# Performance work log

Hardware: AMD Instinct MI355X
Metric: run time of the kernel (lower is better)

## Reference

```python
import jax, jax.numpy as jnp
import numpy as np

N_NODES = 20000
N_EDGES = 640000
BASIS = 128
NUM_GAUSS = 64
HIDDEN = 256
NUM_ATOMS = 100
NUM_GRAPHS = 256
T = 3


def setup_inputs() -> dict:
    key = jax.random.key(0)
    ks = jax.random.split(key, 16)
    Z = jax.random.randint(ks[0], (N_NODES,), 0, NUM_ATOMS + 1)
    edge_index = jax.random.randint(ks[1], (2, N_EDGES), 0, N_NODES)
    edge_attr = jax.random.normal(ks[2], (N_EDGES, NUM_GAUSS), dtype=jnp.float32)
    batch = jnp.sort(jax.random.randint(ks[3], (N_NODES,), 0, NUM_GRAPHS))
    s = 0.05
    embed = jax.random.normal(ks[4], (NUM_ATOMS + 1, BASIS), dtype=jnp.float32)
    cfW = jax.random.normal(ks[5], (BASIS, BASIS), dtype=jnp.float32) * s
    cfb = jax.random.normal(ks[6], (BASIS,), dtype=jnp.float32) * s
    dfW = jax.random.normal(ks[7], (BASIS, NUM_GAUSS), dtype=jnp.float32) * s
    dfb = jax.random.normal(ks[8], (BASIS,), dtype=jnp.float32) * s
    fcW = jax.random.normal(ks[9], (BASIS, BASIS), dtype=jnp.float32) * s
    r1W = jax.random.normal(ks[10], (HIDDEN, BASIS), dtype=jnp.float32) * s
    r1b = jax.random.normal(ks[11], (HIDDEN,), dtype=jnp.float32) * s
    r2W = jax.random.normal(ks[12], (4, HIDDEN), dtype=jnp.float32) * s
    r2b = jax.random.normal(ks[13], (4,), dtype=jnp.float32) * s
    return dict(Z=Z, edge_index=edge_index, edge_attr=edge_attr, batch=batch,
                embed=embed, cfW=cfW, cfb=cfb, dfW=dfW, dfb=dfb, fcW=fcW,
                r1W=r1W, r1b=r1b, r2W=r2W, r2b=r2b)


def reference(Z, edge_index, edge_attr, batch, embed, cfW, cfb, dfW, dfb, fcW,
              r1W, r1b, r2W, r2b):
    # Node embeddings C: [N, basis]
    C = embed[Z]
    src = edge_index[0]  # x_j source nodes
    dst = edge_index[1]  # aggregation target nodes
    # df(edge_attr) is iteration-invariant (shared InteractionBlock weights)
    d_feat = edge_attr @ dfW.T + dfb  # [E, basis]
    for _ in range(T):
        # message: tanh(fc(cf(x_j) * df(edge_attr)))
        c_feat = C[src] @ cfW.T + cfb                 # [E, basis]
        m = jnp.tanh((c_feat * d_feat) @ fcW.T)       # [E, basis]
        agg = jax.ops.segment_sum(m, dst, num_segments=N_NODES)
        C = C + agg
    # readout MLP: Linear -> tanh -> Linear
    h = jnp.tanh(C @ r1W.T + r1b) @ r2W.T + r2b       # [N, 4]
    # global_add_pool over graphs
    return jax.ops.segment_sum(h, batch, num_segments=NUM_GRAPHS)  # [G, 4]
```

## Files before the change

### kernel.cpp

```cpp
#include <hip/hip_runtime.h>
#include <cstdint>

#define NN 20000
#define NE 640000
#define NB 128
#define NG 64
#define NH 256

typedef __attribute__((ext_vector_type(8))) short bf16x8;
typedef __attribute__((ext_vector_type(4))) float f32x4;
typedef __attribute__((ext_vector_type(4))) float fvec4;
typedef __attribute__((ext_vector_type(4))) unsigned uvec4;

__device__ __forceinline__ unsigned fbits(float f){ union{float f; unsigned u;} v; v.f=f; return v.u; }
__device__ __forceinline__ float ubits(unsigned u){ union{unsigned u; float f;} v; v.u=u; return v.f; }

__device__ __forceinline__ unsigned pkf(float a, float b){
  return __builtin_amdgcn_perm(fbits(b)+0x8000u, fbits(a)+0x8000u, 0x07060302u);
}
__device__ __forceinline__ unsigned mulbb(unsigned c, unsigned d){
  float lo = ubits(c << 16) * ubits(d << 16);
  float hi = ubits(c & 0xFFFF0000u) * ubits(d & 0xFFFF0000u);
  return pkf(lo, hi);
}
__device__ __forceinline__ short f2bf_fast(float f){ return (short)((fbits(f)+0x8000u)>>16); }

__device__ __forceinline__ float tanh_fast(float x){
  float t = __builtin_amdgcn_exp2f(x * 2.8853900817779268f);
  return __builtin_fmaf(-2.f, __builtin_amdgcn_rcpf(t + 1.f), 1.f);
}

template<int NT, int KT>
__device__ __forceinline__ void stage_w(const float* __restrict__ W, short* lds){
  const int total = NT*KT*64;
  for(int c = (int)threadIdx.x; c < total; c += 256){
    int lane = c & 63;
    int kt = (c >> 6) % KT;
    int n  = c / (64*KT);
    int row = n*16 + (lane & 15);
    int col = kt*32 + (lane >> 4)*8;
    const float* p = W + (size_t)row*(KT*32) + col;
    unsigned* d = (unsigned*)(lds + (size_t)c*8);
#pragma unroll
    for(int j=0;j<4;j++) d[j] = pkf(p[2*j], p[2*j+1]);
  }
}

__global__ void k_prep0(const int* __restrict__ Z, const float* __restrict__ E,
                        float* __restrict__ C, const int* __restrict__ dst, int* __restrict__ cnt){
  int i = blockIdx.x*256 + threadIdx.x;
  int node = i >> 5, k4 = i & 31;
  ((float4*)C)[i] = ((const float4*)(E + (size_t)Z[node]*NB))[k4];
  atomicAdd(&cnt[dst[i]], 1);
}

__global__ __launch_bounds__(1024) void k_scan(const int* __restrict__ cnt, int* __restrict__ cur){
  __shared__ int lds[1024];
  const int t = threadIdx.x;
  const int base = t*20;
  int4 v[5];
#pragma unroll
  for(int j=0;j<5;j++) v[j] = ((const int4*)(cnt + base))[j];
  const int* ve = (const int*)v;
  int loc[20]; int s = 0;
#pragma unroll
  for(int j=0;j<20;j++){ int c = (base+j < NN) ? ve[j] : 0; loc[j] = s; s += c; }
  lds[t] = s;
  __syncthreads();
  for(int off=1; off<1024; off<<=1){
    int x = (t >= off) ? lds[t-off] : 0;
    __syncthreads();
    lds[t] += x;
    __syncthreads();
  }
  int prefix = (t > 0) ? lds[t-1] : 0;
#pragma unroll
  for(int j=0;j<20;j++){ int i = base+j; if(i<NN) cur[i] = prefix + loc[j]; }
}

__global__ void k_fill(const int* __restrict__ src, const int* __restrict__ dst,
                       int* __restrict__ cur, int* __restrict__ perm,
                       int* __restrict__ srcv, int* __restrict__ dstv){
  int e = blockIdx.x*256 + threadIdx.x;
  if(e < NE){
    int v = dst[e];
    int p = atomicAdd(&cur[v], 1);
    perm[p] = e;
    srcv[p] = src[e];
    dstv[p] = v;
  }
}

#define TPAD 136
__global__ __launch_bounds__(256,3) void k_dprep(
  const float* __restrict__ ea, const int* __restrict__ perm,
  const float* __restrict__ dfW, const float* __restrict__ dfb, short* __restrict__ dft)
{
  __shared__ short ldsW[8*2*64*8];
  __shared__ short ldsT[4*32*TPAD];
  stage_w<8,2>(dfW, ldsW);
  __syncthreads();
  const int lane = threadIdx.x & 63, wave = threadIdx.x >> 6;
  const int quad = lane>>4, lc = lane&15;
  short* myT = ldsT + wave*32*TPAD;
  const int tile0 = (blockIdx.x*4 + wave)*2;

  float bias[8];
#pragma unroll
  for(int n2=0;n2<8;n2++) bias[n2] = dfb[n2*16 + lc];

  int eA[2], eB[2];
#pragma unroll
  for(int mt=0;mt<2;mt++){
    eA[mt] = perm[ tile0   *32 + mt*16 + lc];
    eB[mt] = perm[(tile0+1)*32 + mt*16 + lc];
  }

  fvec4 rA[2][2][2];
#pragma unroll
  for(int mt=0;mt<2;mt++){
    const float* p = ea + (size_t)eA[mt]*NG;
#pragma unroll
    for(int kt=0;kt<2;kt++){
      const float* q = p + kt*32 + quad*8;
      rA[mt][kt][0] = __builtin_nontemporal_load((const fvec4*)q);
      rA[mt][kt][1] = __builtin_nontemporal_load((const fvec4*)(q+4));
    }
  }

  f32x4 z = {0.f,0.f,0.f,0.f};

  auto convert_mfma = [&](fvec4 (&raw)[2][2][2], f32x4 (&acc)[2][8]){
#pragma unroll
    for(int mt=0;mt<2;mt++)
#pragma unroll
      for(int n2=0;n2<8;n2++) acc[mt][n2] = z;
#pragma unroll
    for(int kt=0;kt<2;kt++){
      bf16x8 a0, a1;
      {
        union{ bf16x8 v; unsigned u[4]; } t0, t1;
        fvec4 c0 = raw[0][kt][0], c1 = raw[0][kt][1];
        fvec4 d0 = raw[1][kt][0], d1 = raw[1][kt][1];
        t0.u[0]=pkf(c0.x,c0.y); t0.u[1]=pkf(c0.z,c0.w); t0.u[2]=pkf(c1.x,c1.y); t0.u[3]=pkf(c1.z,c1.w);
        t1.u[0]=pkf(d0.x,d0.y); t1.u[1]=pkf(d0.z,d0.w); t1.u[2]=pkf(d1.x,d1.y); t1.u[3]=pkf(d1.z,d1.w);
        a0 = t0.v; a1 = t1.v;
      }
#pragma unroll
      for(int n2=0;n2<8;n2++){
        bf16x8 b = *(const bf16x8*)(ldsW + ((size_t)(n2*2+kt)*64 + lane)*8);
        acc[0][n2] = __builtin_amdgcn_mfma_f32_16x16x32_bf16(a0, b, acc[0][n2], 0, 0, 0);
        acc[1][n2] = __builtin_amdgcn_mfma_f32_16x16x32_bf16(a1, b, acc[1][n2], 0, 0, 0);
      }
    }
  };

  auto store_tile = [&](f32x4 (&acc)[2][8], int tile){
#pragma unroll
    for(int n2=0;n2<8;n2++)
#pragma unroll
      for(int mt=0;mt<2;mt++)
#pragma unroll
        for(int r=0;r<4;r++)
          myT[(mt*16 + quad*4 + r)*TPAD + n2*16 + lc] = f2bf_fast(acc[mt][n2][r] + bias[n2]);
    short* gout = dft + (size_t)tile*32*NB;
#pragma unroll
    for(int i=0;i<8;i++){
      int s_ = i*512 + lane*8;
      int row = s_ >> 7, col = s_ & 127;
      uvec4 vv = *(const uvec4*)(myT + row*TPAD + col);
      __builtin_nontemporal_store(vv, (uvec4*)(gout + s_));
    }
  };

  f32x4 accA[2][8];
  convert_mfma(rA, accA);

  fvec4 rB[2][2][2];
#pragma unroll
  for(int mt=0;mt<2;mt++){
    const float* p = ea + (size_t)eB[mt]*NG;
#pragma unroll
    for(int kt=0;kt<2;kt++){
      const float* q = p + kt*32 + quad*8;
      rB[mt][kt][0] = __builtin_nontemporal_load((const fvec4*)q);
      rB[mt][kt][1] = __builtin_nontemporal_load((const fvec4*)(q+4));
    }
  }

  store_tile(accA, tile0);

  f32x4 accB[2][8];
  convert_mfma(rB, accB);
  store_tile(accB, tile0+1);
}

__global__ __launch_bounds__(256,3) void k_cf(
  const float* __restrict__ C, const float* __restrict__ cfW,
  const float* __restrict__ cfb, short* __restrict__ cfC)
{
  __shared__ short ldsW[8*4*64*8];
  __shared__ short ldsT[4*16*TPAD];
  stage_w<8,4>(cfW, ldsW);
  __syncthreads();
  const int lane = threadIdx.x & 63, wave = threadIdx.x >> 6;
  const int quad = lane>>4, lc = lane&15;
  short* myT = ldsT + wave*16*TPAD;
  const int tile = blockIdx.x*4 + wave;
  if(tile >= NN/16) return;
  const int base = tile*16;
  bf16x8 a[4];
  const float* p = C + (size_t)(base + lc)*NB;
#pragma unroll
  for(int kt=0;kt<4;kt++){
    const float* q = p + kt*32 + quad*8;
    float4 c0 = *(const float4*)q, c1 = *(const float4*)(q+4);
    union{ bf16x8 v; unsigned u[4]; } t;
    t.u[0]=pkf(c0.x,c0.y); t.u[1]=pkf(c0.z,c0.w); t.u[2]=pkf(c1.x,c1.y); t.u[3]=pkf(c1.z,c1.w);
    a[kt] = t.v;
  }
  f32x4 acc[8];
  f32x4 z = {0.f,0.f,0.f,0.f};
#pragma unroll
  for(int n2=0;n2<8;n2++) acc[n2] = z;
#pragma unroll
  for(int kt=0;kt<4;kt++)
#pragma unroll
    for(int n2=0;n2<8;n2++){
      bf16x8 b = *(const bf16x8*)(ldsW + ((size_t)(n2*4+kt)*64 + lane)*8);
      acc[n2] = __builtin_amdgcn_mfma_f32_16x16x32_bf16(a[kt], b, acc[n2], 0, 0, 0);
    }
#pragma unroll
  for(int n2=0;n2<8;n2++){
    float bias = cfb[n2*16 + lc];
#pragma unroll
    for(int r=0;r<4;r++)
      myT[(quad*4 + r)*TPAD + n2*16 + lc] = f2bf_fast(acc[n2][r] + bias);
  }
  short* gout = cfC + (size_t)base*NB;
#pragma unroll
  for(int i=0;i<4;i++){
    int s_ = i*512 + lane*8;
    int row = s_ >> 7, col = s_ & 127;
    uint4 vv = *(const uint4*)(myT + row*TPAD + col);
    *(uint4*)(gout + s_) = vv;
  }
}

#define ETPW 4
__global__ __launch_bounds__(256,2) void k_edge(
    const short* __restrict__ cfC, const short* __restrict__ dft,
    const int* __restrict__ srcv, const int* __restrict__ dstv,
    const float* __restrict__ fcW, float* __restrict__ C)
{
  __shared__ short ldsW[8*4*64*8];
  stage_w<8,4>(fcW, ldsW);
  __syncthreads();
  const int lane = threadIdx.x & 63, wave = threadIdx.x >> 6;
  const int quad = lane>>4, lc = lane&15;
  const int tile0 = (blockIdx.x*4 + wave)*ETPW;

  int   sv[2][2];
  int   dv[2];
  uint4 cc[2][2][4];
  uint4 dd[2][2][4];

  {
    const int base = tile0*32;
#pragma unroll
    for(int mt=0;mt<2;mt++) sv[0][mt] = srcv[base + mt*16 + lc];
    dv[0] = dstv[base + (lane&31)];
#pragma unroll
    for(int mt=0;mt<2;mt++){
      const short* dp = dft + (size_t)(base + mt*16 + lc)*NB;
#pragma unroll
      for(int kt=0;kt<4;kt++) dd[0][mt][kt] = *(const uint4*)(dp + kt*32 + quad*8);
    }
#pragma unroll
    for(int mt=0;mt<2;mt++){
      const short* cp = cfC + (size_t)sv[0][mt]*NB;
#pragma unroll
      for(int kt=0;kt<4;kt++) cc[0][mt][kt] = *(const uint4*)(cp + kt*32 + quad*8);
    }
  }

#pragma unroll
  for(int t=0; t<ETPW; t++){
    const int cur = t & 1, nxt = cur ^ 1;

    if(t+1 < ETPW){
      const int nbase = (tile0 + t + 1)*32;
#pragma unroll
      for(int mt=0;mt<2;mt++) sv[nxt][mt] = srcv[nbase + mt*16 + lc];
      dv[nxt] = dstv[nbase + (lane&31)];
#pragma unroll
      for(int mt=0;mt<2;mt++){
        const short* dp = dft + (size_t)(nbase + mt*16 + lc)*NB;
#pragma unroll
        for(int kt=0;kt<4;kt++) dd[nxt][mt][kt] = *(const uint4*)(dp + kt*32 + quad*8);
      }
    }

    f32x4 acc[2][8];
    f32x4 z = {0.f,0.f,0.f,0.f};
#pragma unroll
    for(int mt=0;mt<2;mt++)
#pragma unroll
      for(int n2=0;n2<8;n2++) acc[mt][n2] = z;
#pragma unroll
    for(int kt=0;kt<4;kt++){
      bf16x8 a0, a1;
      {
        union{ bf16x8 v; unsigned u[4]; } t0, t1;
        uint4 c0 = cc[cur][0][kt], d0 = dd[cur][0][kt];
        uint4 c1 = cc[cur][1][kt], d1 = dd[cur][1][kt];
        t0.u[0] = mulbb(c0.x, d0.x); t0.u[1] = mulbb(c0.y, d0.y);
        t0.u[2] = mulbb(c0.z, d0.z); t0.u[3] = mulbb(c0.w, d0.w);
        t1.u[0] = mulbb(c1.x, d1.x); t1.u[1] = mulbb(c1.y, d1.y);
        t1.u[2] = mulbb(c1.z, d1.z); t1.u[3] = mulbb(c1.w, d1.w);
        a0 = t0.v; a1 = t1.v;
      }
#pragma unroll
      for(int n2=0;n2<8;n2++){
        bf16x8 b = *(const bf16x8*)(ldsW + ((size_t)(n2*4 + kt)*64 + lane)*8);
        acc[0][n2] = __builtin_amdgcn_mfma_f32_16x16x32_bf16(a0, b, acc[0][n2], 0, 0, 0);
        acc[1][n2] = __builtin_amdgcn_mfma_f32_16x16x32_bf16(a1, b, acc[1][n2], 0, 0, 0);
      }
    }

    if(t+1 < ETPW){
#pragma unroll
      for(int mt=0;mt<2;mt++){
        const short* cp = cfC + (size_t)sv[nxt][mt]*NB;
#pragma unroll
        for(int kt=0;kt<4;kt++) cc[nxt][mt][kt] = *(const uint4*)(cp + kt*32 + quad*8);
      }
    }

#pragma unroll
    for(int mt=0;mt<2;mt++)
#pragma unroll
      for(int n2=0;n2<8;n2++)
#pragma unroll
        for(int r=0;r<4;r++) acc[mt][n2][r] = tanh_fast(acc[mt][n2][r]);

    const int i = lane & 31;
    const int di = dv[cur];
    const int dshift = __shfl_up(di, 1);
    const int dprev = (i > 0) ? dshift : -1;
    unsigned long long mm = __ballot(di != dprev) & 0xFFFFFFFFull;
    while(mm){
      int lo = __ffsll(mm) - 1;
      mm &= mm - 1;
      int hi = mm ? (__ffsll(mm) - 1) : 32;
      int v = __shfl(di, lo);
      float sums[8];
#pragma unroll
      for(int n2=0;n2<8;n2++) sums[n2] = 0.f;
#pragma unroll
      for(int mt=0; mt<2; mt++)
#pragma unroll
        for(int r=0; r<4; r++){
          int e2 = mt*16 + quad*4 + r;
          float sel = (e2 >= lo && e2 < hi) ? 1.f : 0.f;
#pragma unroll
          for(int n2=0;n2<8;n2++) sums[n2] = __builtin_fmaf(acc[mt][n2][r], sel, sums[n2]);
        }
#pragma unroll
      for(int n2=0;n2<8;n2++){
        sums[n2] += __shfl_xor(sums[n2], 16);
        sums[n2] += __shfl_xor(sums[n2], 32);
      }
      const int n2w = quad*2;
      atomicAdd(&C[(size_t)v*NB + n2w*16 + lc],     sums[n2w]);
      atomicAdd(&C[(size_t)v*NB + (n2w+1)*16 + lc], sums[n2w+1]);
    }
  }
}

__global__ __launch_bounds__(256,2) void k_readout(
  const float* __restrict__ C, const float* __restrict__ r1W, const float* __restrict__ r1b,
  const float* __restrict__ r2W, const float* __restrict__ r2b,
  const int* __restrict__ batch, float* __restrict__ out)
{
  __shared__ short ldsW[16*4*64*8];
  stage_w<16,4>(r1W, ldsW);
  __syncthreads();
  const int lane = threadIdx.x & 63, wave = threadIdx.x >> 6;
  const int quad = lane>>4, lc = lane&15;
  const int base = (blockIdx.x*4 + wave)*16;
  if(base >= NN) return;
  int node = base + lc; if(node > NN-1) node = NN-1;
  bf16x8 a[4];
  const float* p = C + (size_t)node*NB;
#pragma unroll
  for(int kt=0;kt<4;kt++){
    const float* q = p + kt*32 + quad*8;
    float4 c0 = *(const float4*)q, c1 = *(const float4*)(q+4);
    union{ bf16x8 v; unsigned u[4]; } t;
    t.u[0]=pkf(c0.x,c0.y); t.u[1]=pkf(c0.z,c0.w); t.u[2]=pkf(c1.x,c1.y); t.u[3]=pkf(c1.z,c1.w);
    a[kt] = t.v;
  }
  f32x4 acc[16];
  f32x4 z = {0.f,0.f,0.f,0.f};
#pragma unroll
  for(int nt=0;nt<16;nt++) acc[nt] = z;
#pragma unroll
  for(int kt=0;kt<4;kt++)
#pragma unroll
    for(int nt=0;nt<16;nt++){
      bf16x8 b = *(const bf16x8*)(ldsW + ((size_t)(nt*4+kt)*64 + lane)*8);
      acc[nt] = __builtin_amdgcn_mfma_f32_16x16x32_bf16(a[kt], b, acc[nt], 0, 0, 0);
    }
#pragma unroll
  for(int nt=0;nt<16;nt++){
    float bias = r1b[nt*16 + lc];
#pragma unroll
    for(int r=0;r<4;r++) acc[nt][r] = tanh_fast(acc[nt][r] + bias);
  }
#pragma unroll
  for(int r=0;r<4;r++){
    int nd = base + quad*4 + r;
#pragma unroll
    for(int o=0;o<4;o++){
      float ps = 0.f;
#pragma unroll
      for(int nt=0;nt<16;nt++) ps = __builtin_fmaf(acc[nt][r], r2W[(size_t)o*NH + nt*16 + lc], ps);
      ps += __shfl_xor(ps, 1);
      ps += __shfl_xor(ps, 2);
      ps += __shfl_xor(ps, 4);
      ps += __shfl_xor(ps, 8);
      if(lc == 0 && nd < NN) atomicAdd(&out[batch[nd]*4 + o], ps + r2b[o]);
    }
  }
}

extern "C" void kernel_launch(void* const* d_in, const int* in_sizes, int n_in,
                              void* d_out, int out_size, void* d_ws, size_t ws_size,
                              hipStream_t stream) {
  const int*   Z      = (const int*)d_in[0];
  const int*   ei     = (const int*)d_in[1];
  const float* ea     = (const float*)d_in[2];
  const int*   batch  = (const int*)d_in[3];
  const float* embedW = (const float*)d_in[4];
  const float* cfW    = (const float*)d_in[5];
  const float* cfb    = (const float*)d_in[6];
  const float* dfW    = (const float*)d_in[7];
  const float* dfb    = (const float*)d_in[8];
  const float* fcW    = (const float*)d_in[9];
  const float* r1W    = (const float*)d_in[10];
  const float* r1b    = (const float*)d_in[11];
  const float* r2W    = (const float*)d_in[12];
  const float* r2b    = (const float*)d_in[13];
  const int* src = ei;
  const int* dst = ei + NE;

  char* p = (char*)d_ws;
  auto alloc = [&](size_t b){ char* r = p; p += (b + 255) & ~(size_t)255; return r; };
  float* CA    = (float*)alloc((size_t)NN*NB*4);
  short* cfC   = (short*)alloc((size_t)NN*NB*2);
  short* dft   = (short*)alloc((size_t)NE*NB*2);
  int*   cnt   = (int*)alloc((size_t)NN*4);
  int*   cursor= (int*)alloc((size_t)NN*4);
  int*   perm  = (int*)alloc((size_t)NE*4);
  int*   srcv  = (int*)alloc((size_t)NE*4);
  int*   dstv  = (int*)alloc((size_t)NE*4);
  size_t needed = (size_t)(p - (char*)d_ws);

  (void)hipMemsetAsync(d_out, 0, (size_t)out_size*sizeof(float), stream);
  if(needed > ws_size) return;

  (void)hipMemsetAsync(cnt, 0, (size_t)NN*4, stream);
  k_prep0<<<2500, 256, 0, stream>>>(Z, embedW, CA, dst, cnt);
  k_scan <<<1,   1024, 0, stream>>>(cnt, cursor);
  k_fill <<<2500, 256, 0, stream>>>(src, dst, cursor, perm, srcv, dstv);
  k_dprep<<<2500, 256, 0, stream>>>(ea, perm, dfW, dfb, dft);

  for(int it = 0; it < 3; it++){
    k_cf  <<<313,  256, 0, stream>>>(CA, cfW, cfb, cfC);
    k_edge<<<1250, 256, 0, stream>>>(cfC, dft, srcv, dstv, fcW, CA);
  }
  k_readout<<<313, 256, 0, stream>>>(CA, r1W, r1b, r2W, r2b, batch, (float*)d_out);
}
```

Before: 666.1 us.

## Switch bf16 MFMA path to fp16 with packed multiply and merged src/dst index array

Converts all intermediate edge/node features and weights from bf16 to fp16, using the hardware pack-convert and v_pk_mul_f16 in place of the manual bf16 multiply emulation, and fp16 MFMA instructions. It also merges the separate src and dst index arrays into one int2 array loaded once per tile and redistributed with shuffles, and raises the edge kernel occupancy hint from 2 to 3 blocks. The goal is to cut ALU work in the edge message inner loop and reduce index loads. fp16 has a narrower range than bf16, so large activations could overflow.

```diff
diff --git a/kernel.cpp b/kernel.cpp
--- a/kernel.cpp
+++ b/kernel.cpp
@@ -7,23 +7,27 @@
 #define NG 64
 #define NH 256
 
-typedef __attribute__((ext_vector_type(8))) short bf16x8;
+typedef __attribute__((ext_vector_type(8))) _Float16 h16x8;
 typedef __attribute__((ext_vector_type(4))) float f32x4;
 typedef __attribute__((ext_vector_type(4))) float fvec4;
 typedef __attribute__((ext_vector_type(4))) unsigned uvec4;
 
 __device__ __forceinline__ unsigned fbits(float f){ union{float f; unsigned u;} v; v.f=f; return v.u; }
-__device__ __forceinline__ float ubits(unsigned u){ union{unsigned u; float f;} v; v.u=u; return v.f; }
-
-__device__ __forceinline__ unsigned pkf(float a, float b){
-  return __builtin_amdgcn_perm(fbits(b)+0x8000u, fbits(a)+0x8000u, 0x07060302u);
-}
-__device__ __forceinline__ unsigned mulbb(unsigned c, unsigned d){
-  float lo = ubits(c << 16) * ubits(d << 16);
-  float hi = ubits(c & 0xFFFF0000u) * ubits(d & 0xFFFF0000u);
-  return pkf(lo, hi);
-}
-__device__ __forceinline__ short f2bf_fast(float f){ return (short)((fbits(f)+0x8000u)>>16); }
+
+__device__ __forceinline__ unsigned pkh(float a, float b){
+  auto t = __builtin_amdgcn_cvt_pkrtz(a, b);
+  return __builtin_bit_cast(unsigned, t);
+}
+__device__ __forceinline__ unsigned pkh_rne(float a, float b){
+  union{ _Float16 h[2]; unsigned u; } v;
+  v.h[0] = (_Float16)a; v.h[1] = (_Float16)b; return v.u;
+}
+__device__ __forceinline__ unsigned pkmul(unsigned a, unsigned b){
+  unsigned r; asm("v_pk_mul_f16 %0, %1, %2" : "=v"(r) : "v"(a), "v"(b)); return r;
+}
+__device__ __forceinline__ short f2h(float f){
+  union{ _Float16 h[2]; short s[2]; } v; v.h[0] = (_Float16)f; return v.s[0];
+}
 
 __device__ __forceinline__ float tanh_fast(float x){
   float t = __builtin_amdgcn_exp2f(x * 2.8853900817779268f);
@@ -42,7 +46,7 @@
     const float* p = W + (size_t)row*(KT*32) + col;
     unsigned* d = (unsigned*)(lds + (size_t)c*8);
 #pragma unroll
-    for(int j=0;j<4;j++) d[j] = pkf(p[2*j], p[2*j+1]);
+    for(int j=0;j<4;j++) d[j] = pkh_rne(p[2*j], p[2*j+1]);
   }
 }
 
@@ -80,14 +84,13 @@
 
 __global__ void k_fill(const int* __restrict__ src, const int* __restrict__ dst,
                        int* __restrict__ cur, int* __restrict__ perm,
-                       int* __restrict__ srcv, int* __restrict__ dstv){
+                       int2* __restrict__ sd){
   int e = blockIdx.x*256 + threadIdx.x;
   if(e < NE){
     int v = dst[e];
     int p = atomicAdd(&cur[v], 1);
     perm[p] = e;
-    srcv[p] = src[e];
-    dstv[p] = v;
+    sd[p] = make_int2(src[e], v);
   }
 }
 
@@ -137,20 +140,20 @@
       for(int n2=0;n2<8;n2++) acc[mt][n2] = z;
 #pragma unroll
     for(int kt=0;kt<2;kt++){
-      bf16x8 a0, a1;
+      h16x8 a0, a1;
       {
-        union{ bf16x8 v; unsigned u[4]; } t0, t1;
+        union{ h16x8 v; unsigned u[4]; } t0, t1;
         fvec4 c0 = raw[0][kt][0], c1 = raw[0][kt][1];
         fvec4 d0 = raw[1][kt][0], d1 = raw[1][kt][1];
-        t0.u[0]=pkf(c0.x,c0.y); t0.u[1]=pkf(c0.z,c0.w); t0.u[2]=pkf(c1.x,c1.y); t0.u[3]=pkf(c1.z,c1.w);
-        t1.u[0]=pkf(d0.x,d0.y); t1.u[1]=pkf(d0.z,d0.w); t1.u[2]=pkf(d1.x,d1.y); t1.u[3]=pkf(d1.z,d1.w);
+        t0.u[0]=pkh(c0.x,c0.y); t0.u[1]=pkh(c0.z,c0.w); t0.u[2]=pkh(c1.x,c1.y); t0.u[3]=pkh(c1.z,c1.w);
+        t1.u[0]=pkh(d0.x,d0.y); t1.u[1]=pkh(d0.z,d0.w); t1.u[2]=pkh(d1.x,d1.y); t1.u[3]=pkh(d1.z,d1.w);
         a0 = t0.v; a1 = t1.v;
       }
 #pragma unroll
       for(int n2=0;n2<8;n2++){
-        bf16x8 b = *(const bf16x8*)(ldsW + ((size_t)(n2*2+kt)*64 + lane)*8);
-        acc[0][n2] = __builtin_amdgcn_mfma_f32_16x16x32_bf16(a0, b, acc[0][n2], 0, 0, 0);
-        acc[1][n2] = __builtin_amdgcn_mfma_f32_16x16x32_bf16(a1, b, acc[1][n2], 0, 0, 0);
+        h16x8 b = *(const h16x8*)(ldsW + ((size_t)(n2*2+kt)*64 + lane)*8);
+        acc[0][n2] = __builtin_amdgcn_mfma_f32_16x16x32_f16(a0, b, acc[0][n2], 0, 0, 0);
+        acc[1][n2] = __builtin_amdgcn_mfma_f32_16x16x32_f16(a1, b, acc[1][n2], 0, 0, 0);
       }
     }
   };
@@ -162,7 +165,7 @@
       for(int mt=0;mt<2;mt++)
 #pragma unroll
         for(int r=0;r<4;r++)
-          myT[(mt*16 + quad*4 + r)*TPAD + n2*16 + lc] = f2bf_fast(acc[mt][n2][r] + bias[n2]);
+          myT[(mt*16 + quad*4 + r)*TPAD + n2*16 + lc] = f2h(acc[mt][n2][r] + bias[n2]);
     short* gout = dft + (size_t)tile*32*NB;
 #pragma unroll
     for(int i=0;i<8;i++){
@@ -209,14 +212,14 @@
   const int tile = blockIdx.x*4 + wave;
   if(tile >= NN/16) return;
   const int base = tile*16;
-  bf16x8 a[4];
+  h16x8 a[4];
   const float* p = C + (size_t)(base + lc)*NB;
 #pragma unroll
   for(int kt=0;kt<4;kt++){
     const float* q = p + kt*32 + quad*8;
     float4 c0 = *(const float4*)q, c1 = *(const float4*)(q+4);
-    union{ bf16x8 v; unsigned u[4]; } t;
-    t.u[0]=pkf(c0.x,c0.y); t.u[1]=pkf(c0.z,c0.w); t.u[2]=pkf(c1.x,c1.y); t.u[3]=pkf(c1.z,c1.w);
+    union{ h16x8 v; unsigned u[4]; } t;
+    t.u[0]=pkh(c0.x,c0.y); t.u[1]=pkh(c0.z,c0.w); t.u[2]=pkh(c1.x,c1.y); t.u[3]=pkh(c1.z,c1.w);
     a[kt] = t.v;
   }
   f32x4 acc[8];
@@ -227,15 +230,15 @@
   for(int kt=0;kt<4;kt++)
 #pragma unroll
     for(int n2=0;n2<8;n2++){
-      bf16x8 b = *(const bf16x8*)(ldsW + ((size_t)(n2*4+kt)*64 + lane)*8);
-      acc[n2] = __builtin_amdgcn_mfma_f32_16x16x32_bf16(a[kt], b, acc[n2], 0, 0, 0);
+      h16x8 b = *(const h16x8*)(ldsW + ((size_t)(n2*4+kt)*64 + lane)*8);
+      acc[n2] = __builtin_amdgcn_mfma_f32_16x16x32_f16(a[kt], b, acc[n2], 0, 0, 0);
     }
 #pragma unroll
   for(int n2=0;n2<8;n2++){
     float bias = cfb[n2*16 + lc];
 #pragma unroll
     for(int r=0;r<4;r++)
-      myT[(quad*4 + r)*TPAD + n2*16 + lc] = f2bf_fast(acc[n2][r] + bias);
+      myT[(quad*4 + r)*TPAD + n2*16 + lc] = f2h(acc[n2][r] + bias);
   }
   short* gout = cfC + (size_t)base*NB;
 #pragma unroll
@@ -248,9 +251,9 @@
 }
 
 #define ETPW 4
-__global__ __launch_bounds__(256,2) void k_edge(
+__global__ __launch_bounds__(256,3) void k_edge(
     const short* __restrict__ cfC, const short* __restrict__ dft,
-    const int* __restrict__ srcv, const int* __restrict__ dstv,
+    const int2* __restrict__ sd,
     const float* __restrict__ fcW, float* __restrict__ C)
 {
   __shared__ short ldsW[8*4*64*8];
@@ -267,9 +270,10 @@
 
   {
     const int base = tile0*32;
-#pragma unroll
-    for(int mt=0;mt<2;mt++) sv[0][mt] = srcv[base + mt*16 + lc];
-    dv[0] = dstv[base + (lane&31)];
+    int2 s0 = sd[base + (lane&31)];
+    dv[0] = s0.y;
+    sv[0][0] = __shfl(s0.x, lc);
+    sv[0][1] = __shfl(s0.x, 16 + lc);
 #pragma unroll
     for(int mt=0;mt<2;mt++){
       const short* dp = dft + (size_t)(base + mt*16 + lc)*NB;
@@ -290,9 +294,10 @@
 
     if(t+1 < ETPW){
       const int nbase = (tile0 + t + 1)*32;
-#pragma unroll
-      for(int mt=0;mt<2;mt++) sv[nxt][mt] = srcv[nbase + mt*16 + lc];
-      dv[nxt] = dstv[nbase + (lane&31)];
+      int2 s0 = sd[nbase + (lane&31)];
+      dv[nxt] = s0.y;
+      sv[nxt][0] = __shfl(s0.x, lc);
+      sv[nxt][1] = __shfl(s0.x, 16 + lc);
 #pragma unroll
       for(int mt=0;mt<2;mt++){
         const short* dp = dft + (size_t)(nbase + mt*16 + lc)*NB;
@@ -309,22 +314,22 @@
       for(int n2=0;n2<8;n2++) acc[mt][n2] = z;
 #pragma unroll
     for(int kt=0;kt<4;kt++){
-      bf16x8 a0, a1;
+      h16x8 a0, a1;
       {
-        union{ bf16x8 v; unsigned u[4]; } t0, t1;
+        union{ h16x8 v; unsigned u[4]; } t0, t1;
         uint4 c0 = cc[cur][0][kt], d0 = dd[cur][0][kt];
         uint4 c1 = cc[cur][1][kt], d1 = dd[cur][1][kt];
-        t0.u[0] = mulbb(c0.x, d0.x); t0.u[1] = mulbb(c0.y, d0.y);
-        t0.u[2] = mulbb(c0.z, d0.z); t0.u[3] = mulbb(c0.w, d0.w);
-        t1.u[0] = mulbb(c1.x, d1.x); t1.u[1] = mulbb(c1.y, d1.y);
-        t1.u[2] = mulbb(c1.z, d1.z); t1.u[3] = mulbb(c1.w, d1.w);
+        t0.u[0] = pkmul(c0.x, d0.x); t0.u[1] = pkmul(c0.y, d0.y);
+        t0.u[2] = pkmul(c0.z, d0.z); t0.u[3] = pkmul(c0.w, d0.w);
+        t1.u[0] = pkmul(c1.x, d1.x); t1.u[1] = pkmul(c1.y, d1.y);
+        t1.u[2] = pkmul(c1.z, d1.z); t1.u[3] = pkmul(c1.w, d1.w);
         a0 = t0.v; a1 = t1.v;
       }
 #pragma unroll
       for(int n2=0;n2<8;n2++){
-        bf16x8 b = *(const bf16x8*)(ldsW + ((size_t)(n2*4 + kt)*64 + lane)*8);
-        acc[0][n2] = __builtin_amdgcn_mfma_f32_16x16x32_bf16(a0, b, acc[0][n2], 0, 0, 0);
-        acc[1][n2] = __builtin_amdgcn_mfma_f32_16x16x32_bf16(a1, b, acc[1][n2], 0, 0, 0);
+        h16x8 b = *(const h16x8*)(ldsW + ((size_t)(n2*4 + kt)*64 + lane)*8);
+        acc[0][n2] = __builtin_amdgcn_mfma_f32_16x16x32_f16(a0, b, acc[0][n2], 0, 0, 0);
+        acc[1][n2] = __builtin_amdgcn_mfma_f32_16x16x32_f16(a1, b, acc[1][n2], 0, 0, 0);
       }
     }
 
@@ -391,14 +396,14 @@
   const int base = (blockIdx.x*4 + wave)*16;
   if(base >= NN) return;
   int node = base + lc; if(node > NN-1) node = NN-1;
-  bf16x8 a[4];
+  h16x8 a[4];
   const float* p = C + (size_t)node*NB;
 #pragma unroll
   for(int kt=0;kt<4;kt++){
     const float* q = p + kt*32 + quad*8;
     float4 c0 = *(const float4*)q, c1 = *(const float4*)(q+4);
-    union{ bf16x8 v; unsigned u[4]; } t;
-    t.u[0]=pkf(c0.x,c0.y); t.u[1]=pkf(c0.z,c0.w); t.u[2]=pkf(c1.x,c1.y); t.u[3]=pkf(c1.z,c1.w);
+    union{ h16x8 v; unsigned u[4]; } t;
+    t.u[0]=pkh(c0.x,c0.y); t.u[1]=pkh(c0.z,c0.w); t.u[2]=pkh(c1.x,c1.y); t.u[3]=pkh(c1.z,c1.w);
     a[kt] = t.v;
   }
   f32x4 acc[16];
@@ -409,8 +414,8 @@
   for(int kt=0;kt<4;kt++)
 #pragma unroll
     for(int nt=0;nt<16;nt++){
-      bf16x8 b = *(const bf16x8*)(ldsW + ((size_t)(nt*4+kt)*64 + lane)*8);
-      acc[nt] = __builtin_amdgcn_mfma_f32_16x16x32_bf16(a[kt], b, acc[nt], 0, 0, 0);
+      h16x8 b = *(const h16x8*)(ldsW + ((size_t)(nt*4+kt)*64 + lane)*8);
+      acc[nt] = __builtin_amdgcn_mfma_f32_16x16x32_f16(a[kt], b, acc[nt], 0, 0, 0);
     }
 #pragma unroll
   for(int nt=0;nt<16;nt++){
@@ -463,8 +468,7 @@
   int*   cnt   = (int*)alloc((size_t)NN*4);
   int*   cursor= (int*)alloc((size_t)NN*4);
   int*   perm  = (int*)alloc((size_t)NE*4);
-  int*   srcv  = (int*)alloc((size_t)NE*4);
-  int*   dstv  = (int*)alloc((size_t)NE*4);
+  int2*  sd    = (int2*)alloc((size_t)NE*8);
   size_t needed = (size_t)(p - (char*)d_ws);
 
   (void)hipMemsetAsync(d_out, 0, (size_t)out_size*sizeof(float), stream);
@@ -473,12 +477,12 @@
   (void)hipMemsetAsync(cnt, 0, (size_t)NN*4, stream);
   k_prep0<<<2500, 256, 0, stream>>>(Z, embedW, CA, dst, cnt);
   k_scan <<<1,   1024, 0, stream>>>(cnt, cursor);
-  k_fill <<<2500, 256, 0, stream>>>(src, dst, cursor, perm, srcv, dstv);
+  k_fill <<<2500, 256, 0, stream>>>(src, dst, cursor, perm, sd);
   k_dprep<<<2500, 256, 0, stream>>>(ea, perm, dfW, dfb, dft);
 
   for(int it = 0; it < 3; it++){
     k_cf  <<<313,  256, 0, stream>>>(CA, cfW, cfb, cfC);
-    k_edge<<<1250, 256, 0, stream>>>(cfC, dft, srcv, dstv, fcW, CA);
+    k_edge<<<1250, 256, 0, stream>>>(cfC, dft, sd, fcW, CA);
   }
   k_readout<<<313, 256, 0, stream>>>(CA, r1W, r1b, r2W, r2b, batch, (float*)d_out);
 }
```

Result: slower. 703.2 us (+5.6%).
